# Kernel optimization log

Hardware: AMD Instinct MI355X
Metric: run time of the kernel (lower is better)

## Reference

```python
import jax, jax.numpy as jnp
import numpy as np

B, T, H, W = 2, 4, 32, 32
DINO_DIM, COG_DIM, NUM_HEADS = 768, 1920, 12
HEAD_DIM = DINO_DIM // NUM_HEADS


def _layernorm(x, g, b, eps=1e-5):
    mu = jnp.mean(x, axis=-1, keepdims=True)
    var = jnp.mean(jnp.square(x - mu), axis=-1, keepdims=True)
    return (x - mu) * jax.lax.rsqrt(var + eps) * g + b


def setup_inputs() -> dict:
    key = jax.random.key(0)
    ks = jax.random.split(key, 12)
    s_d = 1.0 / np.sqrt(DINO_DIM)
    s_c = 1.0 / np.sqrt(COG_DIM)
    return {
        "dino_query": jax.random.normal(ks[0], (B, DINO_DIM, H, W), jnp.float32),
        "cogvideo_keys": jax.random.normal(ks[1], (B, T, H, W, COG_DIM), jnp.float32),
        "temporal_weights": jax.random.uniform(ks[2], (T,), jnp.float32),
        "Wq": jax.random.normal(ks[3], (DINO_DIM, DINO_DIM), jnp.float32) * s_d,
        "bq": jnp.zeros((DINO_DIM,), jnp.float32),
        "Wk": jax.random.normal(ks[4], (COG_DIM, DINO_DIM), jnp.float32) * s_c,
        "bk": jnp.zeros((DINO_DIM,), jnp.float32),
        "Wv": jax.random.normal(ks[5], (COG_DIM, DINO_DIM), jnp.float32) * s_c,
        "bv": jnp.zeros((DINO_DIM,), jnp.float32),
        "Wo": jax.random.normal(ks[6], (DINO_DIM, DINO_DIM), jnp.float32) * s_d,
        "bo": jnp.zeros((DINO_DIM,), jnp.float32),
        "gq": jnp.ones((DINO_DIM,), jnp.float32),
        "Bq": jnp.zeros((DINO_DIM,), jnp.float32),
        "gkv": jnp.ones((COG_DIM,), jnp.float32),
        "Bkv": jnp.zeros((COG_DIM,), jnp.float32),
    }


def reference(dino_query, cogvideo_keys, temporal_weights,
              Wq, bq, Wk, bk, Wv, bv, Wo, bo, gq, Bq, gkv, Bkv):
    b, c, h, w = dino_query.shape
    t = cogvideo_keys.shape[1]
    hw, tkv = h * w, t * cogvideo_keys.shape[2] * cogvideo_keys.shape[3]

    # [B,C,H,W] -> [B,H,W,C]; project after LayerNorm
    xq = _layernorm(jnp.transpose(dino_query, (0, 2, 3, 1)), gq, Bq)
    xkv = _layernorm(cogvideo_keys, gkv, Bkv)
    q = xq @ Wq + bq                      # [B,H,W,C]
    k = xkv @ Wk + bk                     # [B,T,Hk,Wk,C]
    v = xkv @ Wv + bv

    q = q.reshape(b, hw, NUM_HEADS, HEAD_DIM).transpose(0, 2, 1, 3)    # [B,nh,HW,hd]
    k = k.reshape(b, tkv, NUM_HEADS, HEAD_DIM).transpose(0, 2, 1, 3)   # [B,nh,TKV,hd]
    v = v.reshape(b, tkv, NUM_HEADS, HEAD_DIM).transpose(0, 2, 1, 3)

    scores = jnp.einsum('bnqd,bnkd->bnqk', q, k) / np.sqrt(HEAD_DIM)   # [B,nh,HW,TKV]
    # per-key temporal weight: each of the T frames contributes HW keys
    w_key = jnp.repeat(temporal_weights, tkv // t)                     # [TKV]
    scores = scores * w_key[None, None, None, :]
    probs = jax.nn.softmax(scores, axis=-1)

    out = jnp.einsum('bnqk,bnkd->bnqd', probs, v)                      # [B,nh,HW,hd]
    out = out.transpose(0, 2, 1, 3).reshape(b, h, w, c)
    out = out @ Wo + bo
    return jnp.transpose(out, (0, 3, 1, 2))                            # [B,C,H,W]
```

## Files before the change

kernel.cpp:

```cpp
#include <hip/hip_runtime.h>
#include <hip/hip_bf16.h>
#include <math.h>

#define BB   2
#define HWl  1024
#define DINO 768
#define COG  1920
#define NHh  12
#define TKV  4096
#define MQ   (BB*HWl)
#define MKV  (BB*TKV)
#define NSPL 4
#define ROWS_PER_SPLIT (BB*NHh*HWl)

typedef __attribute__((ext_vector_type(8))) short bf16x8;
typedef __attribute__((ext_vector_type(4))) float f32x4;

__device__ __forceinline__ unsigned short f2bf_bits(float f) {
    __hip_bfloat16 h = __float2bfloat16(f);
    return *reinterpret_cast<unsigned short*>(&h);
}

__device__ __forceinline__ void glds16(const __hip_bfloat16* g, __hip_bfloat16* l) {
    __builtin_amdgcn_global_load_lds((const __attribute__((address_space(1))) void*)g,
                                     (__attribute__((address_space(3))) void*)l, 16, 0, 0);
}

__global__ __launch_bounds__(256) void prep1(const float* __restrict__ dino,
                                             const float* __restrict__ cog,
                                             const float* __restrict__ gkv, const float* __restrict__ Bkv,
                                             const float* __restrict__ Wq, const float* __restrict__ Wk,
                                             const float* __restrict__ Wv, const float* __restrict__ Wo,
                                             float* __restrict__ xqT,
                                             __hip_bfloat16* __restrict__ xkv,
                                             __hip_bfloat16* WqT, __hip_bfloat16* WkvT, __hip_bfloat16* WoT) {
    int bid = blockIdx.x, tid = threadIdx.x;
    if (bid < 2048) {
        const int W = COG, W4 = W >> 2, NC = 8;
        int row = bid * 4 + (tid >> 6), lane = tid & 63;
        const float4* xr = (const float4*)(cog + (size_t)row * W);
        const float4* g4 = (const float4*)gkv;
        const float4* b4 = (const float4*)Bkv;
        float4 v[NC];
        float s = 0.f, ss = 0.f;
        #pragma unroll
        for (int i = 0; i < NC; ++i) {
            int c = lane + i * 64;
            float4 t = (c < W4) ? xr[c] : (float4){0.f, 0.f, 0.f, 0.f};
            v[i] = t;
            s  += t.x + t.y + t.z + t.w;
            ss += t.x * t.x + t.y * t.y + t.z * t.z + t.w * t.w;
        }
        #pragma unroll
        for (int off = 1; off < 64; off <<= 1) {
            s  += __shfl_xor(s, off);
            ss += __shfl_xor(ss, off);
        }
        float mu = s / W;
        float rstd = rsqrtf(ss / W - mu * mu + 1e-5f);
        ushort4* yr = (ushort4*)(xkv + (size_t)row * W);
        #pragma unroll
        for (int i = 0; i < NC; ++i) {
            int c = lane + i * 64;
            if (c < W4) {
                float4 t = v[i];
                float4 gg = g4[c], bb = b4[c];
                ushort4 o;
                o.x = f2bf_bits((t.x - mu) * rstd * gg.x + bb.x);
                o.y = f2bf_bits((t.y - mu) * rstd * gg.y + bb.y);
                o.z = f2bf_bits((t.z - mu) * rstd * gg.z + bb.z);
                o.w = f2bf_bits((t.w - mu) * rstd * gg.w + bb.w);
                yr[c] = o;
            }
        }
    } else if (bid < 2432) {
        int t = bid - 2048;
        int h0 = (t & 15) * 64;
        int c0 = ((t >> 4) % 12) * 64;
        int b = t / 192;
        __shared__ float T[64][65];
        #pragma unroll
        for (int i = 0; i < 16; ++i) {
            int idx = tid + i * 256;
            int c = idx >> 6, h = idx & 63;
            T[c][h] = dino[((size_t)b * DINO + c0 + c) * HWl + h0 + h];
        }
        __syncthreads();
        #pragma unroll
        for (int i = 0; i < 16; ++i) {
            int idx = tid + i * 256;
            int r = idx >> 6, c = idx & 63;
            xqT[((size_t)b * HWl + h0 + r) * DINO + c0 + c] = T[c][r];
        }
    } else {
        int bid2 = bid - 2432;
        int mid = bid2 / 1440, r = bid2 % 1440;
        int k0 = (r % 60) * 32, n0 = (r / 60) * 32;
        const float* src = (mid == 0) ? Wq : (mid == 1) ? Wk : (mid == 2) ? Wv : Wo;
        __hip_bfloat16* dst;
        int rowoff = 0;
        if (mid == 0) dst = WqT;
        else if (mid == 1) dst = WkvT;
        else if (mid == 2) { dst = WkvT; rowoff = 768; }
        else dst = WoT;
        int K = (mid == 1 || mid == 2) ? COG : DINO;
        if (k0 >= K) return;
        __shared__ float T[32][33];
        #pragma unroll
        for (int i = 0; i < 4; ++i) {
            int idx = tid + i * 256;
            int rr = idx >> 5, c = idx & 31;
            T[rr][c] = src[(size_t)(k0 + rr) * DINO + n0 + c];
        }
        __syncthreads();
        #pragma unroll
        for (int i = 0; i < 4; ++i) {
            int idx = tid + i * 256;
            int rr = idx >> 5, c = idx & 31;
            dst[(size_t)(rowoff + n0 + rr) * K + k0 + c] = __float2bfloat16(T[c][rr]);
        }
    }
}

__global__ __launch_bounds__(256) void prep2(const float* __restrict__ x,
                                             const float* __restrict__ g,
                                             const float* __restrict__ be,
                                             __hip_bfloat16* __restrict__ y) {
    const int W = DINO, NC = 3;
    int row = blockIdx.x * 4 + (threadIdx.x >> 6);
    int lane = threadIdx.x & 63;
    const float4* xr = (const float4*)(x + (size_t)row * W);
    const float4* g4 = (const float4*)g;
    const float4* b4 = (const float4*)be;
    float4 v[NC];
    float s = 0.f, ss = 0.f;
    #pragma unroll
    for (int i = 0; i < NC; ++i) {
        int c = lane + i * 64;
        float4 t = xr[c];
        v[i] = t;
        s  += t.x + t.y + t.z + t.w;
        ss += t.x * t.x + t.y * t.y + t.z * t.z + t.w * t.w;
    }
    #pragma unroll
    for (int off = 1; off < 64; off <<= 1) {
        s  += __shfl_xor(s, off);
        ss += __shfl_xor(ss, off);
    }
    float mu = s / W;
    float rstd = rsqrtf(ss / W - mu * mu + 1e-5f);
    ushort4* yr = (ushort4*)(y + (size_t)row * W);
    #pragma unroll
    for (int i = 0; i < NC; ++i) {
        int c = lane + i * 64;
        float4 t = v[i];
        float4 gg = g4[c], bb = b4[c];
        ushort4 o;
        o.x = f2bf_bits((t.x - mu) * rstd * gg.x + bb.x);
        o.y = f2bf_bits((t.y - mu) * rstd * gg.y + bb.y);
        o.z = f2bf_bits((t.z - mu) * rstd * gg.z + bb.z);
        o.w = f2bf_bits((t.w - mu) * rstd * gg.w + bb.w);
        yr[c] = o;
    }
}

__global__ __launch_bounds__(256) void stage1(const __hip_bfloat16* __restrict__ xq,
                                              const __hip_bfloat16* __restrict__ WqT,
                                              const float* __restrict__ bq,
                                              __hip_bfloat16* __restrict__ qb,
                                              const __hip_bfloat16* __restrict__ xkv,
                                              const __hip_bfloat16* __restrict__ WkvT,
                                              const float* __restrict__ bk,
                                              const float* __restrict__ bv,
                                              __hip_bfloat16* __restrict__ kb,
                                              __hip_bfloat16* __restrict__ VT) {
    __shared__ __hip_bfloat16 SM[2 * 128 * 64];
    int bid = blockIdx.x;
    int tid = threadIdx.x, w = tid >> 6, lane = tid & 63;
    int l4 = lane & 15, lq = lane >> 4;
    int sws = l4 & 7;
    int rr = tid >> 3;
    int gcs = (tid & 7) ^ (rr & 7);

    if (bid >= 192) {
        const int K = COG;
        __hip_bfloat16* As = SM;
        __hip_bfloat16* Bs = SM + 128 * 64;
        int bidk = bid - 192;
        int m0 = (bidk & 63) * 128, n0 = (bidk >> 6) * 128;
        int mq = (w & 1) * 64, nq = (w >> 1) * 64;
        f32x4 acc[4][4];
        #pragma unroll
        for (int i = 0; i < 4; ++i)
            #pragma unroll
            for (int j = 0; j < 4; ++j) acc[i][j] = (f32x4){0.f, 0.f, 0.f, 0.f};

        const __hip_bfloat16* ag = xkv  + (size_t)(m0 + rr) * K + gcs * 8;
        const __hip_bfloat16* bg = WkvT + (size_t)(n0 + rr) * K + gcs * 8;
        __hip_bfloat16* asl = As + (w * 8) * 64;
        __hip_bfloat16* bsl = Bs + (w * 8) * 64;

        for (int k0 = 0; k0 < K; k0 += 64) {
            __syncthreads();
            #pragma unroll
            for (int g = 0; g < 4; ++g) {
                glds16(ag + (size_t)(g * 32) * K + k0, asl + g * 32 * 64);
                glds16(bg + (size_t)(g * 32) * K + k0, bsl + g * 32 * 64);
            }
            __syncthreads();
            #pragma unroll
            for (int h = 0; h < 2; ++h) {
                bf16x8 a[4], b[4];
                #pragma unroll
                for (int i = 0; i < 4; ++i)
                    a[i] = *(const bf16x8*)(As + (mq + 16 * i + l4) * 64 + (((h * 4 + lq) ^ sws) * 8));
                #pragma unroll
                for (int j = 0; j < 4; ++j)
                    b[j] = *(const bf16x8*)(Bs + (nq + 16 * j + l4) * 64 + (((h * 4 + lq) ^ sws) * 8));
                #pragma unroll
                for (int i = 0; i < 4; ++i)
                    #pragma unroll
                    for (int j = 0; j < 4; ++j)
                        acc[i][j] = __builtin_amdgcn_mfma_f32_16x16x32_bf16(a[i], b[j], acc[i][j], 0, 0, 0);
            }
        }

        if (n0 < 768) {
            #pragma unroll
            for (int i = 0; i < 4; ++i)
                #pragma unroll
                for (int j = 0; j < 4; ++j)
                    #pragma unroll
                    for (int r = 0; r < 4; ++r) {
                        int m = m0 + mq + 16 * i + lq * 4 + r;
                        int n = n0 + nq + 16 * j + l4;
                        kb[(size_t)m * DINO + n] = __float2bfloat16(acc[i][j][r] + bk[n]);
                    }
        } else {
            #pragma unroll
            for (int i = 0; i < 4; ++i)
                #pragma unroll
                for (int j = 0; j < 4; ++j)
                    #pragma unroll
                    for (int r = 0; r < 4; ++r) {
                        int m = m0 + mq + 16 * i + lq * 4 + r;
                        int n = n0 + nq + 16 * j + l4 - 768;
                        VT[((size_t)((m >> 12) * 768 + n)) * TKV + (m & 4095)] =
                            __float2bfloat16(acc[i][j][r] + bv[n]);
                    }
        }
    } else {
        const int K = DINO;
        __hip_bfloat16* As = SM;
        __hip_bfloat16* Bs = SM + 64 * 64;
        int m0 = (bid & 31) * 64, n0 = (bid >> 5) * 128;
        int mq = (w & 1) * 32, nq = (w >> 1) * 64;
        f32x4 acc[2][4];
        #pragma unroll
        for (int i = 0; i < 2; ++i)
            #pragma unroll
            for (int j = 0; j < 4; ++j) acc[i][j] = (f32x4){0.f, 0.f, 0.f, 0.f};

        const __hip_bfloat16* ag = xq  + (size_t)(m0 + rr) * K + gcs * 8;
        const __hip_bfloat16* bg = WqT + (size_t)(n0 + rr) * K + gcs * 8;
        __hip_bfloat16* asl = As + (w * 8) * 64;
        __hip_bfloat16* bsl = Bs + (w * 8) * 64;

        for (int k0 = 0; k0 < K; k0 += 64) {
            __syncthreads();
            #pragma unroll
            for (int g = 0; g < 2; ++g)
                glds16(ag + (size_t)(g * 32) * K + k0, asl + g * 32 * 64);
            #pragma unroll
            for (int g = 0; g < 4; ++g)
                glds16(bg + (size_t)(g * 32) * K + k0, bsl + g * 32 * 64);
            __syncthreads();
            #pragma unroll
            for (int h = 0; h < 2; ++h) {
                bf16x8 a[2], b[4];
                #pragma unroll
                for (int i = 0; i < 2; ++i)
                    a[i] = *(const bf16x8*)(As + (mq + 16 * i + l4) * 64 + (((h * 4 + lq) ^ sws) * 8));
                #pragma unroll
                for (int j = 0; j < 4; ++j)
                    b[j] = *(const bf16x8*)(Bs + (nq + 16 * j + l4) * 64 + (((h * 4 + lq) ^ sws) * 8));
                #pragma unroll
                for (int i = 0; i < 2; ++i)
                    #pragma unroll
                    for (int j = 0; j < 4; ++j)
                        acc[i][j] = __builtin_amdgcn_mfma_f32_16x16x32_bf16(a[i], b[j], acc[i][j], 0, 0, 0);
            }
        }
        #pragma unroll
        for (int i = 0; i < 2; ++i)
            #pragma unroll
            for (int j = 0; j < 4; ++j)
                #pragma unroll
                for (int r = 0; r < 4; ++r) {
                    int m = m0 + mq + 16 * i + lq * 4 + r;
                    int n = n0 + nq + 16 * j + l4;
                    qb[(size_t)m * DINO + n] = __float2bfloat16(acc[i][j][r] + bq[n]);
                }
    }
}

__global__ __launch_bounds__(256) void gemm_o(const __hip_bfloat16* __restrict__ A,
                                              const __hip_bfloat16* __restrict__ Bt,
                                              const float* __restrict__ bias,
                                              float* __restrict__ out) {
    const int K = DINO;
    __shared__ __hip_bfloat16 As[64 * 64];
    __shared__ __hip_bfloat16 Bs[64 * 64];
    int m0 = blockIdx.x * 64, n0 = blockIdx.y * 64;
    int tid = threadIdx.x, w = tid >> 6, lane = tid & 63;
    int l4 = lane & 15, lq = lane >> 4;
    int mq = (w & 1) * 32, nq = (w >> 1) * 32;
    f32x4 acc[2][2];
    #pragma unroll
    for (int i = 0; i < 2; ++i)
        #pragma unroll
        for (int j = 0; j < 2; ++j) acc[i][j] = (f32x4){0.f, 0.f, 0.f, 0.f};

    int rr = tid >> 3;
    int gc = (tid & 7) ^ (rr & 7);
    const __hip_bfloat16* ag = A  + (size_t)(m0 + rr) * K + gc * 8;
    const __hip_bfloat16* bg = Bt + (size_t)(n0 + rr) * K + gc * 8;
    __hip_bfloat16* asl = As + (w * 8) * 64;
    __hip_bfloat16* bsl = Bs + (w * 8) * 64;
    int sws = l4 & 7;

    for (int k0 = 0; k0 < K; k0 += 64) {
        __syncthreads();
        #pragma unroll
        for (int g = 0; g < 2; ++g) {
            glds16(ag + (size_t)(g * 32) * K + k0, asl + g * 32 * 64);
            glds16(bg + (size_t)(g * 32) * K + k0, bsl + g * 32 * 64);
        }
        __syncthreads();
        #pragma unroll
        for (int h = 0; h < 2; ++h) {
            bf16x8 a[2], b[2];
            #pragma unroll
            for (int i = 0; i < 2; ++i)
                a[i] = *(const bf16x8*)(As + (mq + 16 * i + l4) * 64 + (((h * 4 + lq) ^ sws) * 8));
            #pragma unroll
            for (int j = 0; j < 2; ++j)
                b[j] = *(const bf16x8*)(Bs + (nq + 16 * j + l4) * 64 + (((h * 4 + lq) ^ sws) * 8));
            #pragma unroll
            for (int i = 0; i < 2; ++i)
                #pragma unroll
                for (int j = 0; j < 2; ++j)
                    acc[i][j] = __builtin_amdgcn_mfma_f32_16x16x32_bf16(b[j], a[i], acc[i][j], 0, 0, 0);
        }
    }
    #pragma unroll
    for (int i = 0; i < 2; ++i)
        #pragma unroll
        for (int j = 0; j < 2; ++j)
            #pragma unroll
            for (int r = 0; r < 4; ++r) {
                int n = n0 + nq + 16 * j + lq * 4 + r;
                int m = m0 + mq + 16 * i + l4;
                int b = m >> 10, hw = m & 1023;
                out[((size_t)b * DINO + n) * HWl + hw] = acc[i][j][r] + bias[n];
            }
}

__global__ __launch_bounds__(256) void attn4(const __hip_bfloat16* __restrict__ qb,
                                             const __hip_bfloat16* __restrict__ kb,
                                             const __hip_bfloat16* __restrict__ VT,
                                             const float* __restrict__ tw,
                                             __hip_bfloat16* __restrict__ Opart,
                                             float* __restrict__ lpart) {
    int bid = blockIdx.x;
    int g = bid % 96, qc = bid / 96;
    int s = g & 3, bh = g >> 2;
    int head = bh % NHh, b = bh / NHh;
    int tid = threadIdx.x, w = tid >> 6, lane = tid & 63;
    int l4 = lane & 15, lq = lane >> 4;

    __shared__ __hip_bfloat16 Ks[2 * 64 * 64];
    __shared__ __hip_bfloat16 Vs[2 * 64 * 64];
    __shared__ __hip_bfloat16 Ps[4 * 32 * 64];

    const __hip_bfloat16* qbase = qb + (size_t)(b * HWl + qc * 128 + w * 32 + l4) * DINO + head * 64;
    bf16x8 qA0 = *(const bf16x8*)(qbase + lq * 8);
    bf16x8 qA1 = *(const bf16x8*)(qbase + 32 + lq * 8);
    const __hip_bfloat16* qbase2 = qbase + (size_t)16 * DINO;
    bf16x8 qB0 = *(const bf16x8*)(qbase2 + lq * 8);
    bf16x8 qB1 = *(const bf16x8*)(qbase2 + 32 + lq * 8);

    float c = tw[s] * 0.125f * 1.44269504f;
    float l_iA = 0.f, l_iB = 0.f;
    f32x4 oA[4], oB[4];
    #pragma unroll
    for (int j = 0; j < 4; ++j) { oA[j] = (f32x4){0.f,0.f,0.f,0.f}; oB[j] = (f32x4){0.f,0.f,0.f,0.f}; }

    int rowA = w * 16 + (lane >> 3);
    int cg = (lane & 7) ^ ((lane >> 3) & 7);
    const __hip_bfloat16* kg0 = kb + (size_t)(b * TKV + s * 1024 + rowA) * DINO + head * 64 + cg * 8;
    const __hip_bfloat16* kg1 = kg0 + (size_t)8 * DINO;
    const __hip_bfloat16* vg0 = VT + (size_t)(b * 768 + head * 64 + rowA) * TKV + s * 1024 + cg * 8;
    const __hip_bfloat16* vg1 = vg0 + (size_t)8 * TKV;
    int klo0 = (w * 2 + 0) * 512, klo1 = (w * 2 + 1) * 512;

    int sw0 = (lq ^ (l4 & 7)) * 8;
    int sw1 = ((4 + lq) ^ (l4 & 7)) * 8;
    __hip_bfloat16* PsA = Ps + w * 2048 + l4 * 64;
    __hip_bfloat16* PsB = Ps + w * 2048 + (16 + l4) * 64;

    glds16(kg0, Ks + klo0);
    glds16(kg1, Ks + klo1);
    glds16(vg0, Vs + klo0);
    glds16(vg1, Vs + klo1);

    for (int kt = 0; kt < 16; ++kt) {
        int cur = (kt & 1) * 4096;
        __syncthreads();
        if (kt < 15) {
            int nxt = cur ^ 4096;
            glds16(kg0 + (size_t)(kt + 1) * 64 * DINO, Ks + nxt + klo0);
            glds16(kg1 + (size_t)(kt + 1) * 64 * DINO, Ks + nxt + klo1);
            glds16(vg0 + (kt + 1) * 64, Vs + nxt + klo0);
            glds16(vg1 + (kt + 1) * 64, Vs + nxt + klo1);
        }
        const __hip_bfloat16* Kc = Ks + cur;
        const __hip_bfloat16* Vc = Vs + cur;

        f32x4 stA[4], stB[4];
        #pragma unroll
        for (int j = 0; j < 4; ++j) {
            const __hip_bfloat16* kr = Kc + (16 * j + l4) * 64;
            bf16x8 kf0 = *(const bf16x8*)(kr + sw0);
            bf16x8 kf1 = *(const bf16x8*)(kr + sw1);
            f32x4 a = (f32x4){0.f,0.f,0.f,0.f};
            a = __builtin_amdgcn_mfma_f32_16x16x32_bf16(kf0, qA0, a, 0, 0, 0);
            a = __builtin_amdgcn_mfma_f32_16x16x32_bf16(kf1, qA1, a, 0, 0, 0);
            stA[j] = a;
            f32x4 bb = (f32x4){0.f,0.f,0.f,0.f};
            bb = __builtin_amdgcn_mfma_f32_16x16x32_bf16(kf0, qB0, bb, 0, 0, 0);
            bb = __builtin_amdgcn_mfma_f32_16x16x32_bf16(kf1, qB1, bb, 0, 0, 0);
            stB[j] = bb;
        }

        float lsA = 0.f, lsB = 0.f;
        #pragma unroll
        for (int j = 0; j < 4; ++j)
            #pragma unroll
            for (int r = 0; r < 4; ++r) {
                float eA = exp2f(stA[j][r] * c);
                float eB = exp2f(stB[j][r] * c);
                stA[j][r] = eA; lsA += eA;
                stB[j][r] = eB; lsB += eB;
            }
        lsA += __shfl_xor(lsA, 16); lsA += __shfl_xor(lsA, 32);
        lsB += __shfl_xor(lsB, 16); lsB += __shfl_xor(lsB, 32);
        l_iA += lsA; l_iB += lsB;

        #pragma unroll
        for (int j = 0; j < 4; ++j) {
            int off = (((2 * j + (lq >> 1)) ^ (l4 & 7)) << 3) + (lq & 1) * 4;
            ushort4 pA, pB;
            pA.x = f2bf_bits(stA[j][0]); pA.y = f2bf_bits(stA[j][1]);
            pA.z = f2bf_bits(stA[j][2]); pA.w = f2bf_bits(stA[j][3]);
            pB.x = f2bf_bits(stB[j][0]); pB.y = f2bf_bits(stB[j][1]);
            pB.z = f2bf_bits(stB[j][2]); pB.w = f2bf_bits(stB[j][3]);
            *(ushort4*)&PsA[off] = pA;
            *(ushort4*)&PsB[off] = pB;
        }
        bf16x8 paA0 = *(const bf16x8*)(PsA + sw0);
        bf16x8 paA1 = *(const bf16x8*)(PsA + sw1);
        bf16x8 paB0 = *(const bf16x8*)(PsB + sw0);
        bf16x8 paB1 = *(const bf16x8*)(PsB + sw1);

        #pragma unroll
        for (int j = 0; j < 4; ++j) {
            const __hip_bfloat16* vr = Vc + (16 * j + l4) * 64;
            bf16x8 vf0 = *(const bf16x8*)(vr + sw0);
            bf16x8 vf1 = *(const bf16x8*)(vr + sw1);
            oA[j] = __builtin_amdgcn_mfma_f32_16x16x32_bf16(paA0, vf0, oA[j], 0, 0, 0);
            oA[j] = __builtin_amdgcn_mfma_f32_16x16x32_bf16(paA1, vf1, oA[j], 0, 0, 0);
            oB[j] = __builtin_amdgcn_mfma_f32_16x16x32_bf16(paB0, vf0, oB[j], 0, 0, 0);
            oB[j] = __builtin_amdgcn_mfma_f32_16x16x32_bf16(paB1, vf1, oB[j], 0, 0, 0);
        }
    }

    size_t rb = (size_t)s * ROWS_PER_SPLIT + (size_t)(b * NHh + head) * HWl + qc * 128 + w * 32;
    #pragma unroll
    for (int j = 0; j < 4; ++j)
        #pragma unroll
        for (int r = 0; r < 4; ++r) {
            Opart[(rb + lq * 4 + r) * 64 + j * 16 + l4]      = __float2bfloat16(oA[j][r]);
            Opart[(rb + 16 + lq * 4 + r) * 64 + j * 16 + l4] = __float2bfloat16(oB[j][r]);
        }
    if (lq == 0) {
        lpart[rb + l4]      = l_iA;
        lpart[rb + 16 + l4] = l_iB;
    }
}

__global__ void combine(const __hip_bfloat16* __restrict__ Opart, const float* __restrict__ lpart,
                        __hip_bfloat16* __restrict__ attn) {
    int p = blockIdx.x * 4 + (threadIdx.x >> 6);
    int d = threadIdx.x & 63;
    float L = 0.f, O = 0.f;
    #pragma unroll
    for (int s = 0; s < NSPL; ++s) {
        L += lpart[(size_t)s * ROWS_PER_SPLIT + p];
        O += __bfloat162float(Opart[((size_t)s * ROWS_PER_SPLIT + p) * 64 + d]);
    }
    float res = O / L;
    int q = p & 1023;
    int bh = p >> 10;
    int head = bh % NHh, b = bh / NHh;
    attn[((size_t)(b * HWl + q)) * DINO + head * 64 + d] = __float2bfloat16(res);
}

extern "C" void kernel_launch(void* const* d_in, const int* in_sizes, int n_in,
                              void* d_out, int out_size, void* d_ws, size_t ws_size,
                              hipStream_t stream) {
    (void)in_sizes; (void)n_in; (void)out_size; (void)ws_size;
    const float* dino = (const float*)d_in[0];
    const float* cog  = (const float*)d_in[1];
    const float* tw   = (const float*)d_in[2];
    const float* Wq   = (const float*)d_in[3];
    const float* bq   = (const float*)d_in[4];
    const float* Wk   = (const float*)d_in[5];
    const float* bk   = (const float*)d_in[6];
    const float* Wv   = (const float*)d_in[7];
    const float* bv   = (const float*)d_in[8];
    const float* Wo   = (const float*)d_in[9];
    const float* bo   = (const float*)d_in[10];
    const float* gq   = (const float*)d_in[11];
    const float* Bq   = (const float*)d_in[12];
    const float* gkv  = (const float*)d_in[13];
    const float* Bkv  = (const float*)d_in[14];

    char* p = (char*)d_ws;
    float* xqT = (float*)p;                    p += (size_t)MQ * DINO * 4;
    __hip_bfloat16* xq = (__hip_bfloat16*)p;   p += (size_t)MQ * DINO * 2;
    char* alias = p;                           p += (size_t)MKV * COG * 2;
    __hip_bfloat16* xkv = (__hip_bfloat16*)alias;
    __hip_bfloat16* WqT  = (__hip_bfloat16*)p; p += (size_t)DINO * DINO * 2;
    __hip_bfloat16* WkvT = (__hip_bfloat16*)p; p += (size_t)1536 * COG * 2;
    __hip_bfloat16* WoT  = (__hip_bfloat16*)p; p += (size_t)DINO * DINO * 2;
    __hip_bfloat16* qb   = (__hip_bfloat16*)p; p += (size_t)MQ  * DINO * 2;
    __hip_bfloat16* kb   = (__hip_bfloat16*)p; p += (size_t)MKV * DINO * 2;
    __hip_bfloat16* VT   = (__hip_bfloat16*)p; p += (size_t)MKV * DINO * 2;
    __hip_bfloat16* attnb = (__hip_bfloat16*)p; p += (size_t)MQ * DINO * 2;
    __hip_bfloat16* Opart = (__hip_bfloat16*)alias;
    float* lpart = (float*)(alias + (size_t)NSPL * ROWS_PER_SPLIT * 64 * 2);

    prep1<<<8192, 256, 0, stream>>>(dino, cog, gkv, Bkv,
                                    Wq, Wk, Wv, Wo, xqT, xkv, WqT, WkvT, WoT);
    prep2<<<MQ / 4, 256, 0, stream>>>(xqT, gq, Bq, xq);
    stage1<<<960, 256, 0, stream>>>(xq, WqT, bq, qb, xkv, WkvT, bk, bv, kb, VT);
    attn4<<<BB * NHh * 8 * NSPL, 256, 0, stream>>>(qb, kb, VT, tw, Opart, lpart);
    combine<<<ROWS_PER_SPLIT / 4, 256, 0, stream>>>(Opart, lpart, attnb);
    gemm_o<<<dim3(32, 12), 256, 0, stream>>>(attnb, WoT, bo, (float*)d_out);
}
```

Baseline: 271.3 us.

## Rewrite stage1 GEMM as 256x256 tiles with 8 waves and double-buffered LDS pipeline

```diff
diff --git a/kernel.cpp b/kernel.cpp
--- a/kernel.cpp
+++ b/kernel.cpp
@@ -164,143 +164,155 @@
     }
 }
 
-__global__ __launch_bounds__(256) void stage1(const __hip_bfloat16* __restrict__ xq,
-                                              const __hip_bfloat16* __restrict__ WqT,
-                                              const float* __restrict__ bq,
-                                              __hip_bfloat16* __restrict__ qb,
-                                              const __hip_bfloat16* __restrict__ xkv,
-                                              const __hip_bfloat16* __restrict__ WkvT,
-                                              const float* __restrict__ bk,
-                                              const float* __restrict__ bv,
-                                              __hip_bfloat16* __restrict__ kb,
-                                              __hip_bfloat16* __restrict__ VT) {
-    __shared__ __hip_bfloat16 SM[2 * 128 * 64];
+#define VM4 asm volatile("s_waitcnt vmcnt(4)" ::: "memory")
+#define VM0 asm volatile("s_waitcnt vmcnt(0)" ::: "memory")
+
+#define STAGE_A(d, h, tau) do { \
+    int _o = (aRow + (h) * 64) * Kd + (tau) * 64 + cgo; \
+    __hip_bfloat16* _dp = SM + (d) * 32768 + (h) * 8192 + wido; \
+    glds16(Ag + _o, _dp); \
+    glds16(Ag + _o + 128 * Kd, _dp + 4096); \
+} while (0)
+
+#define STAGE_B(d, h, tau) do { \
+    int _o = (bRow + (h) * 32) * Kd + (tau) * 64 + cgo; \
+    __hip_bfloat16* _dp = SM + (d) * 32768 + 16384 + (h) * 8192 + wido; \
+    glds16(Bg + _o, _dp); \
+    glds16(Bg + _o + 128 * Kd, _dp + 4096); \
+} while (0)
+
+#define PHASE(MH, NH, STAGE_STMT, WAIT_STMT) do { \
+    const __hip_bfloat16* _Ab = SM + cur * 32768 + (MH) * 8192 + aoff; \
+    const __hip_bfloat16* _Bb = SM + cur * 32768 + 16384 + (NH) * 8192 + boff; \
+    bf16x8 _a[4][2], _b[2][2]; \
+    _Pragma("unroll") \
+    for (int i = 0; i < 4; ++i) { \
+        _a[i][0] = *(const bf16x8*)(_Ab + i * 1024 + c0); \
+        _a[i][1] = *(const bf16x8*)(_Ab + i * 1024 + c1); \
+    } \
+    _Pragma("unroll") \
+    for (int j = 0; j < 2; ++j) { \
+        _b[j][0] = *(const bf16x8*)(_Bb + j * 1024 + c0); \
+        _b[j][1] = *(const bf16x8*)(_Bb + j * 1024 + c1); \
+    } \
+    STAGE_STMT; \
+    WAIT_STMT; \
+    __builtin_amdgcn_sched_barrier(0); \
+    __builtin_amdgcn_s_barrier(); \
+    __builtin_amdgcn_sched_barrier(0); \
+    __builtin_amdgcn_s_setprio(1); \
+    _Pragma("unroll") \
+    for (int i = 0; i < 4; ++i) \
+        _Pragma("unroll") \
+        for (int j = 0; j < 2; ++j) { \
+            f32x4 _t = acc[(MH) * 4 + i][(NH) * 2 + j]; \
+            _t = __builtin_amdgcn_mfma_f32_16x16x32_bf16(_a[i][0], _b[j][0], _t, 0, 0, 0); \
+            _t = __builtin_amdgcn_mfma_f32_16x16x32_bf16(_a[i][1], _b[j][1], _t, 0, 0, 0); \
+            acc[(MH) * 4 + i][(NH) * 2 + j] = _t; \
+        } \
+    __builtin_amdgcn_s_setprio(0); \
+    __builtin_amdgcn_sched_barrier(0); \
+    __builtin_amdgcn_s_barrier(); \
+} while (0)
+
+__global__ __launch_bounds__(512, 2) void stage1(const __hip_bfloat16* __restrict__ xq,
+                                                 const __hip_bfloat16* __restrict__ WqT,
+                                                 const float* __restrict__ bq,
+                                                 __hip_bfloat16* __restrict__ qb,
+                                                 const __hip_bfloat16* __restrict__ xkv,
+                                                 const __hip_bfloat16* __restrict__ WkvT,
+                                                 const float* __restrict__ bk,
+                                                 const float* __restrict__ bv,
+                                                 __hip_bfloat16* __restrict__ kb,
+                                                 __hip_bfloat16* __restrict__ VT) {
+    __shared__ __hip_bfloat16 SM[65536];
     int bid = blockIdx.x;
-    int tid = threadIdx.x, w = tid >> 6, lane = tid & 63;
+    int tid = threadIdx.x;
+    int wid = tid >> 6, lane = tid & 63;
     int l4 = lane & 15, lq = lane >> 4;
-    int sws = l4 & 7;
-    int rr = tid >> 3;
-    int gcs = (tid & 7) ^ (rr & 7);
-
-    if (bid >= 192) {
-        const int K = COG;
-        __hip_bfloat16* As = SM;
-        __hip_bfloat16* Bs = SM + 128 * 64;
-        int bidk = bid - 192;
-        int m0 = (bidk & 63) * 128, n0 = (bidk >> 6) * 128;
-        int mq = (w & 1) * 64, nq = (w >> 1) * 64;
-        f32x4 acc[4][4];
-        #pragma unroll
-        for (int i = 0; i < 4; ++i)
-            #pragma unroll
-            for (int j = 0; j < 4; ++j) acc[i][j] = (f32x4){0.f, 0.f, 0.f, 0.f};
-
-        const __hip_bfloat16* ag = xkv  + (size_t)(m0 + rr) * K + gcs * 8;
-        const __hip_bfloat16* bg = WkvT + (size_t)(n0 + rr) * K + gcs * 8;
-        __hip_bfloat16* asl = As + (w * 8) * 64;
-        __hip_bfloat16* bsl = Bs + (w * 8) * 64;
-
-        for (int k0 = 0; k0 < K; k0 += 64) {
-            __syncthreads();
-            #pragma unroll
-            for (int g = 0; g < 4; ++g) {
-                glds16(ag + (size_t)(g * 32) * K + k0, asl + g * 32 * 64);
-                glds16(bg + (size_t)(g * 32) * K + k0, bsl + g * 32 * 64);
+    int wr = wid >> 2, wc = wid & 3;
+    int tr = tid >> 3;
+    int cgo = ((tid & 7) ^ (tr & 7)) * 8;
+    int wido = wid * 512;
+
+    const __hip_bfloat16 *Ag, *Bg;
+    int m0, n0, Kd, NT, isQ;
+    if (bid < 192) {
+        m0 = (bid & 31) * 256; n0 = (bid >> 5) * 256;
+        Ag = xkv; Bg = WkvT; Kd = COG; NT = COG / 64; isQ = 0;
+    } else {
+        int t = bid - 192;
+        m0 = (t & 7) * 256; n0 = (t >> 3) * 256;
+        Ag = xq; Bg = WqT; Kd = DINO; NT = DINO / 64; isQ = 1;
+    }
+
+    const int aRow = m0 + tr;
+    const int bRow = n0 + ((tid >> 8) << 6) + (tr & 31);
+    const int aoff = (wr * 64 + l4) * 64;
+    const int boff = (wc * 32 + l4) * 64;
+    const int c0 = ((lq) ^ (l4 & 7)) * 8;
+    const int c1 = ((4 + lq) ^ (l4 & 7)) * 8;
+
+    f32x4 acc[8][4];
+    #pragma unroll
+    for (int i = 0; i < 8; ++i)
+        #pragma unroll
+        for (int j = 0; j < 4; ++j) acc[i][j] = (f32x4){0.f, 0.f, 0.f, 0.f};
+
+    STAGE_A(0, 0, 0); STAGE_B(0, 0, 0); STAGE_A(0, 1, 0); STAGE_B(0, 1, 0);
+    STAGE_A(1, 0, 1); STAGE_B(1, 0, 1);
+    VM4;
+    __builtin_amdgcn_s_barrier();
+
+    for (int g = 0; g < NT; ++g) {
+        int cur = g & 1, nxt = cur ^ 1;
+        bool s1 = (g + 1 < NT), s2 = (g + 2 < NT);
+        PHASE(0, 0, if (s1) STAGE_A(nxt, 1, g + 1), (void)0);
+        PHASE(1, 0, if (s1) STAGE_B(nxt, 1, g + 1), (void)0);
+        PHASE(0, 1, if (s2) STAGE_B(cur, 0, g + 2), (void)0);
+        PHASE(1, 1, if (s2) STAGE_A(cur, 0, g + 2),
+              if (s2) { VM4; } else { VM0; });
+    }
+
+    if (isQ) {
+        #pragma unroll
+        for (int ii = 0; ii < 8; ++ii)
+            #pragma unroll
+            for (int jj = 0; jj < 4; ++jj) {
+                int m = m0 + wr * 128 + (ii >> 2) * 64 + (ii & 3) * 16 + lq * 4;
+                int n = n0 + wc * 64 + (jj >> 1) * 32 + (jj & 1) * 16 + l4;
+                float bb = bq[n];
+                #pragma unroll
+                for (int r = 0; r < 4; ++r)
+                    qb[(size_t)(m + r) * DINO + n] = __float2bfloat16(acc[ii][jj][r] + bb);
             }
-            __syncthreads();
-            #pragma unroll
-            for (int h = 0; h < 2; ++h) {
-                bf16x8 a[4], b[4];
+    } else if (n0 < 768) {
+        #pragma unroll
+        for (int ii = 0; ii < 8; ++ii)
+            #pragma unroll
+            for (int jj = 0; jj < 4; ++jj) {
+                int m = m0 + wr * 128 + (ii >> 2) * 64 + (ii & 3) * 16 + lq * 4;
+                int n = n0 + wc * 64 + (jj >> 1) * 32 + (jj & 1) * 16 + l4;
+                float bb = bk[n];
                 #pragma unroll
-                for (int i = 0; i < 4; ++i)
-                    a[i] = *(const bf16x8*)(As + (mq + 16 * i + l4) * 64 + (((h * 4 + lq) ^ sws) * 8));
-                #pragma unroll
-                for (int j = 0; j < 4; ++j)
-                    b[j] = *(const bf16x8*)(Bs + (nq + 16 * j + l4) * 64 + (((h * 4 + lq) ^ sws) * 8));
-                #pragma unroll
-                for (int i = 0; i < 4; ++i)
-                    #pragma unroll
-                    for (int j = 0; j < 4; ++j)
-                        acc[i][j] = __builtin_amdgcn_mfma_f32_16x16x32_bf16(a[i], b[j], acc[i][j], 0, 0, 0);
+                for (int r = 0; r < 4; ++r)
+                    kb[(size_t)(m + r) * DINO + n] = __float2bfloat16(acc[ii][jj][r] + bb);
             }
-        }
-
-        if (n0 < 768) {
-            #pragma unroll
-            for (int i = 0; i < 4; ++i)
-                #pragma unroll
-                for (int j = 0; j < 4; ++j)
-                    #pragma unroll
-                    for (int r = 0; r < 4; ++r) {
-                        int m = m0 + mq + 16 * i + lq * 4 + r;
-                        int n = n0 + nq + 16 * j + l4;
-                        kb[(size_t)m * DINO + n] = __float2bfloat16(acc[i][j][r] + bk[n]);
-                    }
-        } else {
-            #pragma unroll
-            for (int i = 0; i < 4; ++i)
-                #pragma unroll
-                for (int j = 0; j < 4; ++j)
-                    #pragma unroll
-                    for (int r = 0; r < 4; ++r) {
-                        int m = m0 + mq + 16 * i + lq * 4 + r;
-                        int n = n0 + nq + 16 * j + l4 - 768;
-                        VT[((size_t)((m >> 12) * 768 + n)) * TKV + (m & 4095)] =
-                            __float2bfloat16(acc[i][j][r] + bv[n]);
-                    }
-        }
     } else {
-        const int K = DINO;
-        __hip_bfloat16* As = SM;
-        __hip_bfloat16* Bs = SM + 64 * 64;
-        int m0 = (bid & 31) * 64, n0 = (bid >> 5) * 128;
-        int mq = (w & 1) * 32, nq = (w >> 1) * 64;
-        f32x4 acc[2][4];
-        #pragma unroll
-        for (int i = 0; i < 2; ++i)
-            #pragma unroll
-            for (int j = 0; j < 4; ++j) acc[i][j] = (f32x4){0.f, 0.f, 0.f, 0.f};
-
-        const __hip_bfloat16* ag = xq  + (size_t)(m0 + rr) * K + gcs * 8;
-        const __hip_bfloat16* bg = WqT + (size_t)(n0 + rr) * K + gcs * 8;
-        __hip_bfloat16* asl = As + (w * 8) * 64;
-        __hip_bfloat16* bsl = Bs + (w * 8) * 64;
-
-        for (int k0 = 0; k0 < K; k0 += 64) {
-            __syncthreads();
-            #pragma unroll
-            for (int g = 0; g < 2; ++g)
-                glds16(ag + (size_t)(g * 32) * K + k0, asl + g * 32 * 64);
-            #pragma unroll
-            for (int g = 0; g < 4; ++g)
-                glds16(bg + (size_t)(g * 32) * K + k0, bsl + g * 32 * 64);
-            __syncthreads();
-            #pragma unroll
-            for (int h = 0; h < 2; ++h) {
-                bf16x8 a[2], b[4];
-                #pragma unroll
-                for (int i = 0; i < 2; ++i)
-                    a[i] = *(const bf16x8*)(As + (mq + 16 * i + l4) * 64 + (((h * 4 + lq) ^ sws) * 8));
-                #pragma unroll
-                for (int j = 0; j < 4; ++j)
-                    b[j] = *(const bf16x8*)(Bs + (nq + 16 * j + l4) * 64 + (((h * 4 + lq) ^ sws) * 8));
-                #pragma unroll
-                for (int i = 0; i < 2; ++i)
-                    #pragma unroll
-                    for (int j = 0; j < 4; ++j)
-                        acc[i][j] = __builtin_amdgcn_mfma_f32_16x16x32_bf16(a[i], b[j], acc[i][j], 0, 0, 0);
-            }
-        }
-        #pragma unroll
-        for (int i = 0; i < 2; ++i)
-            #pragma unroll
-            for (int j = 0; j < 4; ++j)
+        #pragma unroll
+        for (int ii = 0; ii < 8; ++ii)
+            #pragma unroll
+            for (int jj = 0; jj < 4; ++jj) {
+                int m = m0 + wr * 128 + (ii >> 2) * 64 + (ii & 3) * 16 + lq * 4;
+                int nv = n0 - 768 + wc * 64 + (jj >> 1) * 32 + (jj & 1) * 16 + l4;
+                float bb = bv[nv];
                 #pragma unroll
                 for (int r = 0; r < 4; ++r) {
-                    int m = m0 + mq + 16 * i + lq * 4 + r;
-                    int n = n0 + nq + 16 * j + l4;
-                    qb[(size_t)m * DINO + n] = __float2bfloat16(acc[i][j][r] + bq[n]);
+                    int mm = m + r;
+                    VT[((size_t)((mm >> 12) * 768 + nv)) * TKV + (mm & 4095)] =
+                        __float2bfloat16(acc[ii][jj][r] + bb);
                 }
+            }
     }
 }
 
@@ -554,7 +566,7 @@
     prep1<<<8192, 256, 0, stream>>>(dino, cog, gkv, Bkv,
                                     Wq, Wk, Wv, Wo, xqT, xkv, WqT, WkvT, WoT);
     prep2<<<MQ / 4, 256, 0, stream>>>(xqT, gq, Bq, xq);
-    stage1<<<960, 256, 0, stream>>>(xq, WqT, bq, qb, xkv, WkvT, bk, bv, kb, VT);
+    stage1<<<216, 512, 0, stream>>>(xq, WqT, bq, qb, xkv, WkvT, bk, bv, kb, VT);
     attn4<<<BB * NHh * 8 * NSPL, 256, 0, stream>>>(qb, kb, VT, tw, Opart, lpart);
     combine<<<ROWS_PER_SPLIT / 4, 256, 0, stream>>>(Opart, lpart, attnb);
     gemm_o<<<dim3(32, 12), 256, 0, stream>>>(attnb, WoT, bo, (float*)d_out);
```

Measured after the change: 267.6 us. Within noise of the previous version (-1.4%).
